# Optimization experiments

Hardware: AMD Instinct MI355X
Metric: run time of the kernel (lower is better)

The kernel has to match this reference:

```python
import jax, jax.numpy as jnp
import numpy as np

N_NODES = 100000
N_EDGES = 1600000
HIDDEN = 64


def setup_inputs() -> dict:
    key = jax.random.key(0)
    k1, k2, k3, k4 = jax.random.split(key, 4)
    x = jax.random.normal(k1, (N_NODES, HIDDEN), dtype=jnp.float32)
    A_rows = jax.random.randint(k2, (N_EDGES,), 0, N_NODES, dtype=jnp.int32)
    A_cols = jax.random.randint(k3, (N_EDGES,), 0, N_NODES, dtype=jnp.int32)
    A_vals = jax.random.uniform(k4, (N_EDGES,), dtype=jnp.float32)
    t = jnp.zeros((), dtype=jnp.float32)
    return {"t": t, "x": x, "A_rows": A_rows, "A_cols": A_cols, "A_vals": A_vals}


def reference(t, x, A_rows, A_cols, A_vals):
    # f = A @ x  (sparse COO SpMM): gather source features, scale, scatter-add to rows
    msgs = A_vals[:, None] * x[A_cols]           # [E, H]
    f = jax.ops.segment_sum(msgs, A_rows, num_segments=N_NODES)  # [N, H]
    # dropout rate is 0.0 -> identity; then ReLU
    return jax.nn.relu(f)
```

## Files before the change

### kernel.cpp

```cpp
#include <hip/hip_runtime.h>
#include <hip/hip_fp16.h>

#define N_NODES 100000
#define N_EDGES 1600000
#define HIDDEN 64
#define RPB 512
#define NCB ((N_NODES + RPB - 1) / RPB)
#define CAP 8960
#define NPART 256
#define R1_BATCH 4096
#define R1_PER_T (R1_BATCH / 256)


__global__ void __launch_bounds__(256) conv_fp16_kernel(const float4* __restrict__ x4,
                                                        ushort4* __restrict__ xh,
                                                        int n4) {
    int i = blockIdx.x * blockDim.x + threadIdx.x;
    const int stride = gridDim.x * blockDim.x;
    for (; i < n4; i += stride) {
        const float4 v = x4[i];
        ushort4 q;
        q.x = __half_as_ushort(__float2half(v.x));
        q.y = __half_as_ushort(__float2half(v.y));
        q.z = __half_as_ushort(__float2half(v.z));
        q.w = __half_as_ushort(__float2half(v.w));
        xh[i] = q;
    }
}

__global__ void __launch_bounds__(256) coarse_scatter_pad_kernel(
        const int* __restrict__ rows, const int* __restrict__ cols,
        const float* __restrict__ vals, int* __restrict__ ccursor,
        int2* __restrict__ cbuf) {
    __shared__ int hist[NCB];
    __shared__ int base[NCB];
    __shared__ int lcur[NCB];
    const int t = threadIdx.x;
    const int b0 = blockIdx.x * R1_BATCH;
    for (int i = t; i < NCB; i += 256) { hist[i] = 0; lcur[i] = 0; }
    __syncthreads();

    int  mb[R1_PER_T];
    int2 md[R1_PER_T];
    #pragma unroll
    for (int k = 0; k < R1_PER_T; ++k) {
        const int e = b0 + k * 256 + t;
        if (e < N_EDGES) {
            const int r = rows[e];
            mb[k] = r >> 9;
            md[k] = make_int2(((r & 511) << 17) | cols[e], __float_as_int(vals[e]));
            atomicAdd(&hist[mb[k]], 1);
        } else {
            mb[k] = -1;
        }
    }
    __syncthreads();
    for (int i = t; i < NCB; i += 256) {
        const int c = hist[i];
        base[i] = c ? (i * CAP + atomicAdd(&ccursor[i], c)) : 0;
    }
    __syncthreads();
    #pragma unroll
    for (int k = 0; k < R1_PER_T; ++k) {
        if (mb[k] >= 0) {
            const int rank = atomicAdd(&lcur[mb[k]], 1);
            cbuf[base[mb[k]] + rank] = md[k];
        }
    }
}

__global__ void __launch_bounds__(256) count_scan_kernel(const int* __restrict__ ccursor,
                                                         int* __restrict__ cbase,
                                                         int* __restrict__ offs) {
    __shared__ int s[2][256];
    const int t = threadIdx.x;
    s[0][t] = (t < NCB) ? ccursor[t] : 0;
    __syncthreads();
    int src = 0;
    for (int off = 1; off < 256; off <<= 1) {
        s[1 - src][t] = s[src][t] + (t >= off ? s[src][t - off] : 0);
        __syncthreads();
        src ^= 1;
    }
    if (t <= NCB) cbase[t] = t ? s[src][t - 1] : 0;
    if (t == 0) offs[N_NODES] = N_EDGES;
}

__global__ void __launch_bounds__(1024) fine_bucket_pad_kernel(
        const int2* __restrict__ cbuf, const int* __restrict__ cbase,
        int* __restrict__ offs, int2* __restrict__ ebuf) {
    __shared__ int s[2][RPB];
    __shared__ int lcur[RPB];
    const int b = blockIdx.x;
    const int t = threadIdx.x;
    const int rowbase = b << 9;
    const int src0 = b * CAP;
    const int dst0 = cbase[b];
    const int cnt  = cbase[b + 1] - dst0;

    if (t < RPB) s[0][t] = 0;
    __syncthreads();
    for (int i = t; i < cnt; i += 1024)
        atomicAdd(&s[0][cbuf[src0 + i].x >> 17], 1);
    __syncthreads();
    int src = 0;
    for (int off = 1; off < RPB; off <<= 1) {
        if (t < RPB) s[1 - src][t] = s[src][t] + (t >= off ? s[src][t - off] : 0);
        __syncthreads();
        src ^= 1;
    }
    if (t < RPB) {
        const int excl = dst0 + (t ? s[src][t - 1] : 0);
        const int row = rowbase + t;
        if (row < N_NODES) offs[row] = excl;
        lcur[t] = excl;
    }
    __syncthreads();
    for (int i = t; i < cnt; i += 1024) {
        const int2 m = cbuf[src0 + i];
        const int pos = atomicAdd(&lcur[m.x >> 17], 1);
        ebuf[pos] = make_int2(m.x & 0x1FFFF, m.y);
    }
}

__global__ void __launch_bounds__(256) spmm_csr_relu_h4_kernel(
        const ushort4* __restrict__ xh, const int2* __restrict__ ebuf,
        const int* __restrict__ offs, float4* __restrict__ out4) {
    const int lane = threadIdx.x & 63;
    const int g = lane >> 4;
    const int h = lane & 15;
    const int wave = threadIdx.x >> 6;
    const int r = blockIdx.x * 4 + wave;
    if (r >= N_NODES) return;
    const int start = offs[r];
    const int n = offs[r + 1] - start;

    float4 acc = make_float4(0.f, 0.f, 0.f, 0.f);
    for (int base = 0; base < n; base += 64) {
        const int take = min(64, n - base);
        int2 m = make_int2(0, 0);
        if (base + lane < n) m = ebuf[start + base + lane];
        for (int j = 0; j < take; j += 8) {
            const int j0 = j + g;
            const int j1 = j + 4 + g;
            const bool p0 = j0 < take;
            const bool p1 = j1 < take;
            const int   c0r = __shfl(m.x, j0);
            const float v0r = __int_as_float(__shfl(m.y, j0));
            const int   c1r = __shfl(m.x, j1);
            const float v1r = __int_as_float(__shfl(m.y, j1));
            const int   c0 = p0 ? c0r : 0;
            const float v0 = p0 ? v0r : 0.0f;
            const int   c1 = p1 ? c1r : 0;
            const float v1 = p1 ? v1r : 0.0f;
            const ushort4 qa = xh[(size_t)c0 * 16 + h];
            const ushort4 qb = xh[(size_t)c1 * 16 + h];
            acc.x = fmaf(v0, __half2float(__ushort_as_half(qa.x)), acc.x);
            acc.y = fmaf(v0, __half2float(__ushort_as_half(qa.y)), acc.y);
            acc.z = fmaf(v0, __half2float(__ushort_as_half(qa.z)), acc.z);
            acc.w = fmaf(v0, __half2float(__ushort_as_half(qa.w)), acc.w);
            acc.x = fmaf(v1, __half2float(__ushort_as_half(qb.x)), acc.x);
            acc.y = fmaf(v1, __half2float(__ushort_as_half(qb.y)), acc.y);
            acc.z = fmaf(v1, __half2float(__ushort_as_half(qb.z)), acc.z);
            acc.w = fmaf(v1, __half2float(__ushort_as_half(qb.w)), acc.w);
        }
    }
    acc.x += __shfl_xor(acc.x, 16); acc.y += __shfl_xor(acc.y, 16);
    acc.z += __shfl_xor(acc.z, 16); acc.w += __shfl_xor(acc.w, 16);
    acc.x += __shfl_xor(acc.x, 32); acc.y += __shfl_xor(acc.y, 32);
    acc.z += __shfl_xor(acc.z, 32); acc.w += __shfl_xor(acc.w, 32);
    if (lane < 16) {
        float4 o;
        o.x = fmaxf(acc.x, 0.f); o.y = fmaxf(acc.y, 0.f);
        o.z = fmaxf(acc.z, 0.f); o.w = fmaxf(acc.w, 0.f);
        out4[(size_t)r * 16 + h] = o;
    }
}

__global__ void __launch_bounds__(256) spmm_csr_relu_f4_kernel(
        const float4* __restrict__ x4, const int2* __restrict__ ebuf,
        const int* __restrict__ offs, float4* __restrict__ out4) {
    const int lane = threadIdx.x & 63;
    const int g = lane >> 4;
    const int h = lane & 15;
    const int wave = threadIdx.x >> 6;
    const int r = blockIdx.x * 4 + wave;
    if (r >= N_NODES) return;
    const int start = offs[r];
    const int n = offs[r + 1] - start;

    float4 acc = make_float4(0.f, 0.f, 0.f, 0.f);
    for (int base = 0; base < n; base += 64) {
        const int take = min(64, n - base);
        int2 m = make_int2(0, 0);
        if (base + lane < n) m = ebuf[start + base + lane];
        for (int j = 0; j < take; j += 8) {
            const int j0 = j + g;
            const int j1 = j + 4 + g;
            const bool p0 = j0 < take;
            const bool p1 = j1 < take;
            const int   c0 = p0 ? __shfl(m.x, j0) : 0;
            const float v0 = p0 ? __int_as_float(__shfl(m.y, j0)) : 0.0f;
            const int   c1 = p1 ? __shfl(m.x, j1) : 0;
            const float v1 = p1 ? __int_as_float(__shfl(m.y, j1)) : 0.0f;
            const float4 a = x4[(size_t)c0 * 16 + h];
            const float4 bq = x4[(size_t)c1 * 16 + h];
            acc.x = fmaf(v0, a.x, acc.x);  acc.y = fmaf(v0, a.y, acc.y);
            acc.z = fmaf(v0, a.z, acc.z);  acc.w = fmaf(v0, a.w, acc.w);
            acc.x = fmaf(v1, bq.x, acc.x); acc.y = fmaf(v1, bq.y, acc.y);
            acc.z = fmaf(v1, bq.z, acc.z); acc.w = fmaf(v1, bq.w, acc.w);
        }
    }
    acc.x += __shfl_xor(acc.x, 16); acc.y += __shfl_xor(acc.y, 16);
    acc.z += __shfl_xor(acc.z, 16); acc.w += __shfl_xor(acc.w, 16);
    acc.x += __shfl_xor(acc.x, 32); acc.y += __shfl_xor(acc.y, 32);
    acc.z += __shfl_xor(acc.z, 32); acc.w += __shfl_xor(acc.w, 32);
    if (lane < 16) {
        float4 o;
        o.x = fmaxf(acc.x, 0.f); o.y = fmaxf(acc.y, 0.f);
        o.z = fmaxf(acc.z, 0.f); o.w = fmaxf(acc.w, 0.f);
        out4[(size_t)r * 16 + h] = o;
    }
}

__global__ void spmm_scatter_kernel(const float* __restrict__ x,
                                    const int* __restrict__ rows,
                                    const int* __restrict__ cols,
                                    const float* __restrict__ vals,
                                    float* __restrict__ f) {
    const int lane = threadIdx.x & 63;
    const int wave = (blockIdx.x * blockDim.x + threadIdx.x) >> 6;
    const int nWaves = (gridDim.x * blockDim.x) >> 6;
    for (int e = wave; e < N_EDGES; e += nWaves)
        atomicAdd(&f[rows[e] * HIDDEN + lane], vals[e] * x[cols[e] * HIDDEN + lane]);
}
__global__ void relu_inplace_kernel(float4* __restrict__ f, int n4) {
    int i = blockIdx.x * blockDim.x + threadIdx.x;
    const int stride = gridDim.x * blockDim.x;
    for (; i < n4; i += stride) {
        float4 v = f[i];
        v.x = fmaxf(v.x, 0.0f); v.y = fmaxf(v.y, 0.0f);
        v.z = fmaxf(v.z, 0.0f); v.w = fmaxf(v.w, 0.0f);
        f[i] = v;
    }
}

extern "C" void kernel_launch(void* const* d_in, const int* in_sizes, int n_in,
                              void* d_out, int out_size, void* d_ws, size_t ws_size,
                              hipStream_t stream) {
    const float* x    = (const float*)d_in[1];
    const int*   rows = (const int*)d_in[2];
    const int*   cols = (const int*)d_in[3];
    const float* vals = (const float*)d_in[4];
    float* out = (float*)d_out;
    char* ws = (char*)d_ws;

    const size_t ccursor_off = 0;
    const size_t cbase_off   = ccursor_off + (size_t)NCB * 4;
    const size_t offs_off    = cbase_off + (size_t)(NCB + 1) * 4;
    size_t cbuf_off = offs_off + (size_t)(N_NODES + 1) * 4;
    cbuf_off = (cbuf_off + 15) & ~(size_t)15;
    const size_t ebuf_off = cbuf_off + (size_t)NCB * CAP * 8;
    const size_t xh_off   = ebuf_off + (size_t)N_EDGES * 8;
    const size_t ws_t1  = xh_off + (size_t)N_NODES * HIDDEN * 2;
    const size_t ws_t1b = ebuf_off + (size_t)N_EDGES * 8;

    if (ws_size >= ws_t1b) {
        int*  ccursor = (int*)(ws + ccursor_off);
        int*  cbase   = (int*)(ws + cbase_off);
        int*  offs    = (int*)(ws + offs_off);
        int2* cbuf    = (int2*)(ws + cbuf_off);
        int2* ebuf    = (int2*)(ws + ebuf_off);
        const bool fp16_path = (ws_size >= ws_t1);

        hipMemsetAsync(ccursor, 0, (size_t)NCB * 4, stream);
        if (fp16_path) {
            ushort4* xh = (ushort4*)(ws + xh_off);
            conv_fp16_kernel<<<2048, 256, 0, stream>>>((const float4*)x, xh,
                                                       N_NODES * HIDDEN / 4);
        }
        coarse_scatter_pad_kernel<<<(N_EDGES + R1_BATCH - 1) / R1_BATCH, 256, 0, stream>>>(
            rows, cols, vals, ccursor, cbuf);
        count_scan_kernel<<<1, 256, 0, stream>>>(ccursor, cbase, offs);
        fine_bucket_pad_kernel<<<NCB, 1024, 0, stream>>>(cbuf, cbase, offs, ebuf);
        if (fp16_path) {
            const ushort4* xh = (const ushort4*)(ws + xh_off);
            spmm_csr_relu_h4_kernel<<<N_NODES / 4, 256, 0, stream>>>(
                xh, ebuf, offs, (float4*)out);
        } else {
            spmm_csr_relu_f4_kernel<<<N_NODES / 4, 256, 0, stream>>>(
                (const float4*)x, ebuf, offs, (float4*)out);
        }
        return;
    }

    hipMemsetAsync(d_out, 0, (size_t)N_NODES * HIDDEN * sizeof(float), stream);
    spmm_scatter_kernel<<<2048, 256, 0, stream>>>(x, rows, cols, vals, out);
    relu_inplace_kernel<<<2048, 256, 0, stream>>>((float4*)d_out,
                                                  (N_NODES * HIDDEN) / 4);
}
```

Before: 105.3 us.

## Reuse histogram atomic ranks and keep edges in registers across bucketing passes

Both bucketing kernels now take the rank returned by the histogram atomicAdd and hold the edge data in registers. The second pass then writes each edge straight to base+rank, with no second shared-memory atomic pass and, in the fine kernel, no second read of cbuf. The coarse kernel moves to 512 threads with 6144-edge batches. In the fp16 SpMM kernel the inner loop gathers four neighbor rows per step instead of two and drops the bounds predicates, which is safe because padding lanes hold column 0 with value 0. The cost is higher register pressure from the per-thread slot arrays.

```diff
diff --git a/kernel.cpp b/kernel.cpp
--- a/kernel.cpp
+++ b/kernel.cpp
@@ -7,10 +7,10 @@
 #define RPB 512
 #define NCB ((N_NODES + RPB - 1) / RPB)
 #define CAP 8960
-#define NPART 256
-#define R1_BATCH 4096
-#define R1_PER_T (R1_BATCH / 256)
-
+#define R1_THREADS 512
+#define R1_BATCH 6144
+#define R1_PER_T (R1_BATCH / R1_THREADS)
+#define FINE_SLOTS 9
 
 __global__ void __launch_bounds__(256) conv_fp16_kernel(const float4* __restrict__ x4,
                                                         ushort4* __restrict__ xh,
@@ -28,45 +28,40 @@
     }
 }
 
-__global__ void __launch_bounds__(256) coarse_scatter_pad_kernel(
+__global__ void __launch_bounds__(R1_THREADS) coarse_scatter_pad_kernel(
         const int* __restrict__ rows, const int* __restrict__ cols,
         const float* __restrict__ vals, int* __restrict__ ccursor,
         int2* __restrict__ cbuf) {
     __shared__ int hist[NCB];
     __shared__ int base[NCB];
-    __shared__ int lcur[NCB];
     const int t = threadIdx.x;
     const int b0 = blockIdx.x * R1_BATCH;
-    for (int i = t; i < NCB; i += 256) { hist[i] = 0; lcur[i] = 0; }
+    for (int i = t; i < NCB; i += R1_THREADS) hist[i] = 0;
     __syncthreads();
 
     int  mb[R1_PER_T];
+    int  rk[R1_PER_T];
     int2 md[R1_PER_T];
     #pragma unroll
     for (int k = 0; k < R1_PER_T; ++k) {
-        const int e = b0 + k * 256 + t;
+        const int e = b0 + k * R1_THREADS + t;
+        mb[k] = -1;
         if (e < N_EDGES) {
             const int r = rows[e];
             mb[k] = r >> 9;
-            md[k] = make_int2(((r & 511) << 17) | cols[e], __float_as_int(vals[e]));
-            atomicAdd(&hist[mb[k]], 1);
-        } else {
-            mb[k] = -1;
-        }
-    }
-    __syncthreads();
-    for (int i = t; i < NCB; i += 256) {
+            md[k] = make_int2(((r & (RPB - 1)) << 17) | cols[e], __float_as_int(vals[e]));
+            rk[k] = atomicAdd(&hist[mb[k]], 1);
+        }
+    }
+    __syncthreads();
+    for (int i = t; i < NCB; i += R1_THREADS) {
         const int c = hist[i];
         base[i] = c ? (i * CAP + atomicAdd(&ccursor[i], c)) : 0;
     }
     __syncthreads();
     #pragma unroll
-    for (int k = 0; k < R1_PER_T; ++k) {
-        if (mb[k] >= 0) {
-            const int rank = atomicAdd(&lcur[mb[k]], 1);
-            cbuf[base[mb[k]] + rank] = md[k];
-        }
-    }
+    for (int k = 0; k < R1_PER_T; ++k)
+        if (mb[k] >= 0) cbuf[base[mb[k]] + rk[k]] = md[k];
 }
 
 __global__ void __launch_bounds__(256) count_scan_kernel(const int* __restrict__ ccursor,
@@ -87,21 +82,35 @@
 }
 
 __global__ void __launch_bounds__(1024) fine_bucket_pad_kernel(
-        const int2* __restrict__ cbuf, const int* __restrict__ cbase,
-        int* __restrict__ offs, int2* __restrict__ ebuf) {
+        const int2* __restrict__ cbuf, const int* __restrict__ ccursor,
+        const int* __restrict__ cbase, int* __restrict__ offs,
+        int2* __restrict__ ebuf) {
     __shared__ int s[2][RPB];
-    __shared__ int lcur[RPB];
+    __shared__ int lbase[RPB];
     const int b = blockIdx.x;
     const int t = threadIdx.x;
-    const int rowbase = b << 9;
+    const int cnt  = min(ccursor[b], CAP);
     const int src0 = b * CAP;
     const int dst0 = cbase[b];
-    const int cnt  = cbase[b + 1] - dst0;
 
     if (t < RPB) s[0][t] = 0;
     __syncthreads();
-    for (int i = t; i < cnt; i += 1024)
-        atomicAdd(&s[0][cbuf[src0 + i].x >> 17], 1);
+
+    int  rw[FINE_SLOTS];
+    int  rk[FINE_SLOTS];
+    int2 md[FINE_SLOTS];
+    #pragma unroll
+    for (int k = 0; k < FINE_SLOTS; ++k) {
+        const int i = k * 1024 + t;
+        rw[k] = -1;
+        if (i < cnt) {
+            const int2 m = cbuf[src0 + i];
+            const int row = (m.x >> 17) & (RPB - 1);
+            rw[k] = row;
+            md[k] = make_int2(m.x & 0x1FFFF, m.y);
+            rk[k] = atomicAdd(&s[0][row], 1);
+        }
+    }
     __syncthreads();
     int src = 0;
     for (int off = 1; off < RPB; off <<= 1) {
@@ -111,16 +120,14 @@
     }
     if (t < RPB) {
         const int excl = dst0 + (t ? s[src][t - 1] : 0);
-        const int row = rowbase + t;
+        lbase[t] = excl;
+        const int row = (b << 9) + t;
         if (row < N_NODES) offs[row] = excl;
-        lcur[t] = excl;
-    }
-    __syncthreads();
-    for (int i = t; i < cnt; i += 1024) {
-        const int2 m = cbuf[src0 + i];
-        const int pos = atomicAdd(&lcur[m.x >> 17], 1);
-        ebuf[pos] = make_int2(m.x & 0x1FFFF, m.y);
-    }
+    }
+    __syncthreads();
+    #pragma unroll
+    for (int k = 0; k < FINE_SLOTS; ++k)
+        if (rw[k] >= 0) ebuf[lbase[rw[k]] + rk[k]] = md[k];
 }
 
 __global__ void __launch_bounds__(256) spmm_csr_relu_h4_kernel(
@@ -140,21 +147,20 @@
         const int take = min(64, n - base);
         int2 m = make_int2(0, 0);
         if (base + lane < n) m = ebuf[start + base + lane];
-        for (int j = 0; j < take; j += 8) {
-            const int j0 = j + g;
-            const int j1 = j + 4 + g;
-            const bool p0 = j0 < take;
-            const bool p1 = j1 < take;
-            const int   c0r = __shfl(m.x, j0);
-            const float v0r = __int_as_float(__shfl(m.y, j0));
-            const int   c1r = __shfl(m.x, j1);
-            const float v1r = __int_as_float(__shfl(m.y, j1));
-            const int   c0 = p0 ? c0r : 0;
-            const float v0 = p0 ? v0r : 0.0f;
-            const int   c1 = p1 ? c1r : 0;
-            const float v1 = p1 ? v1r : 0.0f;
+        for (int j = 0; j < take; j += 16) {
+            const int i0 = j + g, i1 = j + 4 + g, i2 = j + 8 + g, i3 = j + 12 + g;
+            const int   c0 = __shfl(m.x, i0);
+            const float v0 = __int_as_float(__shfl(m.y, i0));
+            const int   c1 = __shfl(m.x, i1);
+            const float v1 = __int_as_float(__shfl(m.y, i1));
+            const int   c2 = __shfl(m.x, i2);
+            const float v2 = __int_as_float(__shfl(m.y, i2));
+            const int   c3 = __shfl(m.x, i3);
+            const float v3 = __int_as_float(__shfl(m.y, i3));
             const ushort4 qa = xh[(size_t)c0 * 16 + h];
             const ushort4 qb = xh[(size_t)c1 * 16 + h];
+            const ushort4 qc = xh[(size_t)c2 * 16 + h];
+            const ushort4 qd = xh[(size_t)c3 * 16 + h];
             acc.x = fmaf(v0, __half2float(__ushort_as_half(qa.x)), acc.x);
             acc.y = fmaf(v0, __half2float(__ushort_as_half(qa.y)), acc.y);
             acc.z = fmaf(v0, __half2float(__ushort_as_half(qa.z)), acc.z);
@@ -163,6 +169,14 @@
             acc.y = fmaf(v1, __half2float(__ushort_as_half(qb.y)), acc.y);
             acc.z = fmaf(v1, __half2float(__ushort_as_half(qb.z)), acc.z);
             acc.w = fmaf(v1, __half2float(__ushort_as_half(qb.w)), acc.w);
+            acc.x = fmaf(v2, __half2float(__ushort_as_half(qc.x)), acc.x);
+            acc.y = fmaf(v2, __half2float(__ushort_as_half(qc.y)), acc.y);
+            acc.z = fmaf(v2, __half2float(__ushort_as_half(qc.z)), acc.z);
+            acc.w = fmaf(v2, __half2float(__ushort_as_half(qc.w)), acc.w);
+            acc.x = fmaf(v3, __half2float(__ushort_as_half(qd.x)), acc.x);
+            acc.y = fmaf(v3, __half2float(__ushort_as_half(qd.y)), acc.y);
+            acc.z = fmaf(v3, __half2float(__ushort_as_half(qd.z)), acc.z);
+            acc.w = fmaf(v3, __half2float(__ushort_as_half(qd.w)), acc.w);
         }
     }
     acc.x += __shfl_xor(acc.x, 16); acc.y += __shfl_xor(acc.y, 16);
@@ -195,15 +209,12 @@
         int2 m = make_int2(0, 0);
         if (base + lane < n) m = ebuf[start + base + lane];
         for (int j = 0; j < take; j += 8) {
-            const int j0 = j + g;
-            const int j1 = j + 4 + g;
-            const bool p0 = j0 < take;
-            const bool p1 = j1 < take;
-            const int   c0 = p0 ? __shfl(m.x, j0) : 0;
-            const float v0 = p0 ? __int_as_float(__shfl(m.y, j0)) : 0.0f;
-            const int   c1 = p1 ? __shfl(m.x, j1) : 0;
-            const float v1 = p1 ? __int_as_float(__shfl(m.y, j1)) : 0.0f;
-            const float4 a = x4[(size_t)c0 * 16 + h];
+            const int j0 = j + g, j1 = j + 4 + g;
+            const int   c0 = __shfl(m.x, j0);
+            const float v0 = __int_as_float(__shfl(m.y, j0));
+            const int   c1 = __shfl(m.x, j1);
+            const float v1 = __int_as_float(__shfl(m.y, j1));
+            const float4 a  = x4[(size_t)c0 * 16 + h];
             const float4 bq = x4[(size_t)c1 * 16 + h];
             acc.x = fmaf(v0, a.x, acc.x);  acc.y = fmaf(v0, a.y, acc.y);
             acc.z = fmaf(v0, a.z, acc.z);  acc.w = fmaf(v0, a.w, acc.w);
@@ -262,8 +273,8 @@
     cbuf_off = (cbuf_off + 15) & ~(size_t)15;
     const size_t ebuf_off = cbuf_off + (size_t)NCB * CAP * 8;
     const size_t xh_off   = ebuf_off + (size_t)N_EDGES * 8;
+    const size_t ws_t1b = xh_off;
     const size_t ws_t1  = xh_off + (size_t)N_NODES * HIDDEN * 2;
-    const size_t ws_t1b = ebuf_off + (size_t)N_EDGES * 8;
 
     if (ws_size >= ws_t1b) {
         int*  ccursor = (int*)(ws + ccursor_off);
@@ -279,10 +290,10 @@
             conv_fp16_kernel<<<2048, 256, 0, stream>>>((const float4*)x, xh,
                                                        N_NODES * HIDDEN / 4);
         }
-        coarse_scatter_pad_kernel<<<(N_EDGES + R1_BATCH - 1) / R1_BATCH, 256, 0, stream>>>(
-            rows, cols, vals, ccursor, cbuf);
+        coarse_scatter_pad_kernel<<<(N_EDGES + R1_BATCH - 1) / R1_BATCH, R1_THREADS,
+                                    0, stream>>>(rows, cols, vals, ccursor, cbuf);
         count_scan_kernel<<<1, 256, 0, stream>>>(ccursor, cbase, offs);
-        fine_bucket_pad_kernel<<<NCB, 1024, 0, stream>>>(cbuf, cbase, offs, ebuf);
+        fine_bucket_pad_kernel<<<NCB, 1024, 0, stream>>>(cbuf, ccursor, cbase, offs, ebuf);
         if (fp16_path) {
             const ushort4* xh = (const ushort4*)(ws + xh_off);
             spmm_csr_relu_h4_kernel<<<N_NODES / 4, 256, 0, stream>>>(
```

Result: faster. 101.2 us (-3.9%).
